# Kernel optimization log

Hardware: AMD Instinct MI355X
Metric: run time of the kernel (lower is better)

The kernel has to match this reference:

```python
import jax, jax.numpy as jnp
import numpy as np

B, T, D_MODEL, HEAD_DIM = 8, 2048, 1024, 128


def setup_inputs() -> dict:
    key = jax.random.key(0)
    k1, k2, k3, k4 = jax.random.split(key, 4)
    scale = 1.0 / np.sqrt(D_MODEL)
    return {
        "x": jax.random.normal(k1, (B, T, D_MODEL), dtype=jnp.float32),
        "Wq": jax.random.normal(k2, (HEAD_DIM, D_MODEL), dtype=jnp.float32) * scale,
        "Wk": jax.random.normal(k3, (HEAD_DIM, D_MODEL), dtype=jnp.float32) * scale,
        "Wv": jax.random.normal(k4, (HEAD_DIM, D_MODEL), dtype=jnp.float32) * scale,
    }


def reference(x, Wq, Wk, Wv) -> jnp.ndarray:
    # x: [B, T, C]; torch Linear(no bias): y = x @ W.T, W: [head_dim, d_model]
    q = jnp.einsum("btc,hc->bth", x, Wq)  # [B, T, H]
    k = jnp.einsum("btc,hc->bth", x, Wk)
    v = jnp.einsum("btc,hc->bth", x, Wv)
    head_dim = Wq.shape[0]
    scores = jnp.einsum("bqh,bkh->bqk", q, k) / jnp.sqrt(jnp.float32(head_dim))  # [B, T, T]
    T_ = x.shape[1]
    causal = jnp.tril(jnp.ones((T_, T_), dtype=bool))
    scores = jnp.where(causal, scores, -jnp.inf)
    probs = jax.nn.softmax(scores, axis=-1)
    # dropout is identity at inference (eval mode)
    out = jnp.einsum("bqk,bkh->bqh", probs, v)  # [B, T, head_dim]
    return out
```

## Files before the change

kernel.cpp:

```cpp
#include <hip/hip_runtime.h>
#include <hip/hip_bf16.h>
#include <math.h>

#define T_ 2048
#define C_ 1024
#define H_ 128
#define NB 8
#define WN 131072
#define SC 0.08838834764831845f

typedef __attribute__((ext_vector_type(8))) short bf16x8;
typedef __attribute__((ext_vector_type(8))) unsigned short u16x8;
typedef __attribute__((ext_vector_type(4))) float f32x4;

#define MFMA16(a,b,c) __builtin_amdgcn_mfma_f32_16x16x32_bf16((a),(b),(c),0,0,0)

__device__ __forceinline__ unsigned short f2bf(float f) {
    union { float f; unsigned u; } v; v.f = f;
    unsigned r = v.u + 0x7fffu + ((v.u >> 16) & 1u);
    return (unsigned short)(r >> 16);
}
__device__ __forceinline__ float bf2f(unsigned short u) {
    union { unsigned u; float f; } v; v.u = ((unsigned)u) << 16; return v.f;
}
__device__ __forceinline__ unsigned pk2bf(float a, float b) {
    __hip_bfloat162 h = __float22bfloat162_rn(float2{a, b});
    union { __hip_bfloat162 h; unsigned u; } v; v.h = h; return v.u;
}
__device__ __forceinline__ void gld16(void* lds, const void* g) {
    __builtin_amdgcn_global_load_lds(
        (const __attribute__((address_space(1))) unsigned*)g,
        (__attribute__((address_space(3))) unsigned*)lds, 16, 0, 0);
}

__global__ __launch_bounds__(256) void wconv(const float* __restrict__ Wq,
                                             const float* __restrict__ Wk,
                                             const float* __restrict__ Wv,
                                             unsigned short* __restrict__ Wb) {
    int e = (blockIdx.x * 256 + threadIdx.x) * 8;
    int which = e >> 17;
    int off = e & (WN - 1);
    const float* src = (which == 0) ? Wq : (which == 1 ? Wk : Wv);
    float s = (which == 0) ? SC : 1.0f;
    const float4* p = (const float4*)(src + off);
    float4 a = p[0], b = p[1];
    uint4 o = { pk2bf(a.x * s, a.y * s), pk2bf(a.z * s, a.w * s),
                pk2bf(b.x * s, b.y * s), pk2bf(b.z * s, b.w * s) };
    *(uint4*)(Wb + e) = o;
}

__global__ __launch_bounds__(256, 2) void proj(const float* __restrict__ x,
                                               const unsigned short* __restrict__ Wb,
                                               unsigned short* __restrict__ Q,
                                               unsigned short* __restrict__ K,
                                               unsigned short* __restrict__ V) {
    __shared__ unsigned short Xs[2][64][64];
    __shared__ unsigned short Ws[2][192][64];

    const int tid  = threadIdx.x;
    const int wave = tid >> 6, lane = tid & 63;
    const int quad = lane >> 4, l16 = lane & 15;
    const int wm   = wave >> 1, wn = wave & 1;
    const int m0   = (blockIdx.x >> 1) * 64;
    const int n0   = (blockIdx.x & 1) * 192;

    f32x4 acc[2][6];
    #pragma unroll
    for (int i = 0; i < 2; i++)
        #pragma unroll
        for (int j = 0; j < 6; j++) acc[i][j] = {0.f, 0.f, 0.f, 0.f};

    const int xrow = tid >> 2, xcg = tid & 3;
    const float* xg = x + (size_t)(m0 + xrow) * C_ + xcg * 16;
    const int xk = xrow & 7;
    const unsigned short* wg = Wb + (size_t)(n0 + wave * 48 + (lane >> 3)) * C_
                               + (size_t)(((lane & 7) ^ (lane >> 3)) * 8);

    float4 xr0, xr1, xr2, xr3;
    #define ISSUE(buf, kc) do {                                                   \
        _Pragma("unroll")                                                         \
        for (int i = 0; i < 6; i++)                                               \
            gld16(&Ws[buf][wave * 48 + i * 8][0], wg + (size_t)i * 8 * C_ + (kc));\
        const float* xp = xg + (kc);                                              \
        xr0 = *(const float4*)xp;        xr1 = *(const float4*)(xp + 4);          \
        xr2 = *(const float4*)(xp + 8);  xr3 = *(const float4*)(xp + 12);         \
    } while (0)

    #define XWRITE(buf) do {                                                      \
        uint4 u0 = { pk2bf(xr0.x, xr0.y), pk2bf(xr0.z, xr0.w),                    \
                     pk2bf(xr1.x, xr1.y), pk2bf(xr1.z, xr1.w) };                  \
        uint4 u1 = { pk2bf(xr2.x, xr2.y), pk2bf(xr2.z, xr2.w),                    \
                     pk2bf(xr3.x, xr3.y), pk2bf(xr3.z, xr3.w) };                  \
        *(uint4*)&Xs[buf][xrow][((2 * xcg)     ^ xk) * 8] = u0;                   \
        *(uint4*)&Xs[buf][xrow][((2 * xcg + 1) ^ xk) * 8] = u1;                   \
    } while (0)

    ISSUE(0, 0);
    XWRITE(0);
    for (int it = 0; it < 16; it++) {
        __syncthreads();
        const int buf = it & 1;
        if (it < 15) ISSUE(buf ^ 1, (it + 1) * 64);
        const int key = l16 & 7;
        bf16x8 af[2][2];
        #pragma unroll
        for (int kk = 0; kk < 2; kk++)
            #pragma unroll
            for (int mf = 0; mf < 2; mf++)
                af[mf][kk] = *(bf16x8*)&Xs[buf][wm * 32 + mf * 16 + l16]
                                          [((kk * 4 + quad) ^ key) * 8];
        #pragma unroll
        for (int kk = 0; kk < 2; kk++)
            #pragma unroll
            for (int nf = 0; nf < 6; nf++) {
                bf16x8 bq = *(bf16x8*)&Ws[buf][wn * 96 + nf * 16 + l16]
                                         [((kk * 4 + quad) ^ key) * 8];
                acc[0][nf] = MFMA16(af[0][kk], bq, acc[0][nf]);
                acc[1][nf] = MFMA16(af[1][kk], bq, acc[1][nf]);
            }
        if (it < 15) XWRITE(buf ^ 1);
    }
    #undef ISSUE
    #undef XWRITE

    #pragma unroll
    for (int nf = 0; nf < 6; nf++) {
        int nb = n0 + wn * 96 + nf * 16;
        int which = nb >> 7;
        unsigned short* dst = (which == 0) ? Q : (which == 1 ? K : V);
        int c = (nb & 127) + l16;
        #pragma unroll
        for (int mf = 0; mf < 2; mf++)
            #pragma unroll
            for (int r = 0; r < 4; r++)
                dst[(size_t)(m0 + wm * 32 + mf * 16 + quad * 4 + r) * H_ + c] = f2bf(acc[mf][nf][r]);
    }
}

__global__ __launch_bounds__(256, 3) void attn(const unsigned short* __restrict__ Qg,
                                               const unsigned short* __restrict__ Kg,
                                               const unsigned short* __restrict__ Vg,
                                               unsigned short* __restrict__ Ob,
                                               float* __restrict__ Ml) {
    const int bid = blockIdx.x;
    const int b   = bid & 7;
    const int j   = bid >> 3;
    int g = 0;
    while (j >= 2 * (g + 1) * (g + 2)) g++;
    const int within = j - 2 * g * (g + 1);
    const int t = within / (g + 1);
    const int s = within - t * (g + 1);
    const int qt = 4 * g + t;
    const int qbase = qt * 64, kstart = s * 256;
    const int kend  = (kstart + 256 < qbase + 64) ? kstart + 256 : qbase + 64;
    const int niter = (kend - kstart) >> 6;

    __shared__ unsigned short Ks[4][64][32];
    __shared__ unsigned short Vt[128 * 64];
    __shared__ unsigned short Ps[4][16][64];

    const int tid = threadIdx.x, wave = tid >> 6, lane = tid & 63;
    const int quad = lane >> 4, l16 = lane & 15;
    const size_t base = (size_t)b * T_ * H_;

    const unsigned short* ksrc = Kg + base + (size_t)(kstart + (lane >> 2)) * H_ + wave * 32 + (lane & 3) * 8;
    #pragma unroll
    for (int p = 0; p < 4; p++) gld16(&Ks[wave][p * 16][0], ksrc + (size_t)p * 16 * H_);
    const unsigned short* vsrc = Vg + base + (size_t)(kstart + wave * 8 + quad * 2) * H_ + l16 * 8;
    u16x8 vr[2][2];
    vr[0][0] = *(const u16x8*)vsrc;             vr[0][1] = *(const u16x8*)(vsrc + H_);
    vr[1][0] = *(const u16x8*)(vsrc + 32 * H_); vr[1][1] = *(const u16x8*)(vsrc + 33 * H_);

    bf16x8 qf[4];
    const unsigned short* qp = Qg + base + (size_t)(qbase + wave * 16 + l16) * H_ + quad * 8;
    #pragma unroll
    for (int kk = 0; kk < 4; kk++) qf[kk] = *(const bf16x8*)(qp + kk * 32);

    f32x4 o[8];
    #pragma unroll
    for (int i = 0; i < 8; i++) o[i] = {0.f, 0.f, 0.f, 0.f};
    float m_i = -INFINITY, l_i = 0.f;
    const int swz = (l16 & 7) << 3;
    const int qg = qbase + wave * 16 + l16;

    __syncthreads();

    #pragma unroll
    for (int g2 = 0; g2 < 2; g2++) {
        int t0 = wave * 8 + g2 * 32 + quad * 2;
        int t8 = t0 >> 3;
        #pragma unroll
        for (int jj = 0; jj < 8; jj++) {
            int h = l16 * 8 + jj;
            unsigned pk = (unsigned)(unsigned short)vr[g2][0][jj] | ((unsigned)(unsigned short)vr[g2][1][jj] << 16);
            int blk = (t8 ^ (h & 7) ^ ((h >> 3) & 7)) & 7;
            *(unsigned*)&Vt[h * 64 + blk * 8 + (t0 & 7)] = pk;
        }
    }

    for (int kt = 0; ; kt++) {
        const int kbase = kstart + kt * 64;
        f32x4 st[4];
        #pragma unroll
        for (int nf = 0; nf < 4; nf++) st[nf] = {0.f, 0.f, 0.f, 0.f};
        #pragma unroll
        for (int kk = 0; kk < 4; kk++)
            #pragma unroll
            for (int nf = 0; nf < 4; nf++) {
                bf16x8 kfr = *(bf16x8*)&Ks[kk][nf * 16 + l16][quad * 8];
                st[nf] = MFMA16(kfr, qf[kk], st[nf]);
            }
        if (kbase + 64 > qbase) {
            #pragma unroll
            for (int nf = 0; nf < 4; nf++) {
                int kg = kbase + nf * 16 + quad * 4;
                #pragma unroll
                for (int r = 0; r < 4; r++)
                    if (kg + r > qg) st[nf][r] = -INFINITY;
            }
        }
        float mx = st[0][0];
        #pragma unroll
        for (int nf = 0; nf < 4; nf++)
            #pragma unroll
            for (int r = 0; r < 4; r++) mx = fmaxf(mx, st[nf][r]);
        mx = fmaxf(mx, __shfl_xor(mx, 16, 64));
        mx = fmaxf(mx, __shfl_xor(mx, 32, 64));
        float mnew = fmaxf(m_i, mx);
        float al = __expf(m_i - mnew);
        m_i = mnew;
        float rs = 0.f;
        #pragma unroll
        for (int nf = 0; nf < 4; nf++)
            #pragma unroll
            for (int r = 0; r < 4; r++) {
                float e = __expf(st[nf][r] - mnew);
                st[nf][r] = e; rs += e;
            }
        rs += __shfl_xor(rs, 16, 64);
        rs += __shfl_xor(rs, 32, 64);
        l_i = al * l_i + rs;
        #pragma unroll
        for (int nf = 0; nf < 4; nf++) {
            uint2 pk = { pk2bf(st[nf][0], st[nf][1]), pk2bf(st[nf][2], st[nf][3]) };
            *(uint2*)&Ps[wave][l16][(nf * 16 + quad * 4) ^ swz] = pk;
        }
        float a0 = __shfl(al, quad * 4 + 0, 64), a1 = __shfl(al, quad * 4 + 1, 64);
        float a2 = __shfl(al, quad * 4 + 2, 64), a3 = __shfl(al, quad * 4 + 3, 64);
        #pragma unroll
        for (int i = 0; i < 8; i++) {
            o[i][0] *= a0; o[i][1] *= a1; o[i][2] *= a2; o[i][3] *= a3;
        }
        __syncthreads();

        const bool more = (kt + 1 < niter);
        if (more) {
            ksrc += 64 * H_;
            #pragma unroll
            for (int p = 0; p < 4; p++) gld16(&Ks[wave][p * 16][0], ksrc + (size_t)p * 16 * H_);
            vsrc += 64 * H_;
            vr[0][0] = *(const u16x8*)vsrc;             vr[0][1] = *(const u16x8*)(vsrc + H_);
            vr[1][0] = *(const u16x8*)(vsrc + 32 * H_); vr[1][1] = *(const u16x8*)(vsrc + 33 * H_);
        }
        bf16x8 pa0 = *(bf16x8*)&Ps[wave][l16][(quad * 8) ^ swz];
        bf16x8 pa1 = *(bf16x8*)&Ps[wave][l16][(32 + quad * 8) ^ swz];
        #pragma unroll
        for (int nf = 0; nf < 8; nf++) {
            int h = nf * 16 + l16;
            int ex = (h & 7) ^ ((h >> 3) & 7);
            bf16x8 v0 = *(bf16x8*)&Vt[h * 64 + ((quad ^ ex) & 7) * 8];
            bf16x8 v1 = *(bf16x8*)&Vt[h * 64 + (((quad + 4) ^ ex) & 7) * 8];
            o[nf] = MFMA16(pa0, v0, o[nf]);
            o[nf] = MFMA16(pa1, v1, o[nf]);
        }
        if (!more) break;
        __syncthreads();
        #pragma unroll
        for (int g2 = 0; g2 < 2; g2++) {
            int t0 = wave * 8 + g2 * 32 + quad * 2;
            int t8 = t0 >> 3;
            #pragma unroll
            for (int jj = 0; jj < 8; jj++) {
                int h = l16 * 8 + jj;
                unsigned pk = (unsigned)(unsigned short)vr[g2][0][jj] | ((unsigned)(unsigned short)vr[g2][1][jj] << 16);
                int blk = (t8 ^ (h & 7) ^ ((h >> 3) & 7)) & 7;
                *(unsigned*)&Vt[h * 64 + blk * 8 + (t0 & 7)] = pk;
            }
        }
    }

    const int slot = j * NB + b;
    float lq[4];
    #pragma unroll
    for (int r = 0; r < 4; r++) lq[r] = __shfl(l_i, quad * 4 + r, 64);
    const size_t obase = (size_t)slot * 64 * 128;
    #pragma unroll
    for (int r = 0; r < 4; r++) {
        float invl = 1.0f / lq[r];
        #pragma unroll
        for (int nf = 0; nf < 8; nf++)
            Ob[obase + (size_t)(wave * 16 + quad * 4 + r) * 128 + nf * 16 + l16] = f2bf(o[nf][r] * invl);
    }
    if (lane < 16) {
        int ridx = slot * 64 + wave * 16 + l16;
        Ml[ridx * 2]     = m_i;
        Ml[ridx * 2 + 1] = l_i;
    }
}

__global__ __launch_bounds__(256) void merge(const unsigned short* __restrict__ Ob,
                                             const float* __restrict__ Ml,
                                             float* __restrict__ out) {
    const int qt = blockIdx.x, b = blockIdx.y;
    const int g = qt >> 2;
    const int Pq = 2 * g * (g + 1) + (qt & 3) * (g + 1);
    const int ns = g + 1;
    const int tid = threadIdx.x;
    const int row = tid >> 2, c0 = (tid & 3) * 32;

    float mv[8], lv[8], mg = -INFINITY;
    for (int s2 = 0; s2 < ns; s2++) {
        int slot = (Pq + s2) * NB + b;
        mv[s2] = Ml[(slot * 64 + row) * 2];
        lv[s2] = Ml[(slot * 64 + row) * 2 + 1];
        mg = fmaxf(mg, mv[s2]);
    }
    float L = 0.f, w[8];
    for (int s2 = 0; s2 < ns; s2++) { w[s2] = lv[s2] * __expf(mv[s2] - mg); L += w[s2]; }
    float inv = 1.0f / L;

    float accv[32];
    #pragma unroll
    for (int i = 0; i < 32; i++) accv[i] = 0.f;
    for (int s2 = 0; s2 < ns; s2++) {
        int slot = (Pq + s2) * NB + b;
        const unsigned short* op = Ob + ((size_t)(slot * 64 + row)) * 128 + c0;
        #pragma unroll
        for (int cc = 0; cc < 4; cc++) {
            u16x8 v = *(const u16x8*)(op + cc * 8);
            #pragma unroll
            for (int jj = 0; jj < 8; jj++) accv[cc * 8 + jj] += w[s2] * bf2f(v[jj]);
        }
    }
    float* od = out + ((size_t)(b * T_ + qt * 64 + row)) * 128 + c0;
    #pragma unroll
    for (int cc = 0; cc < 8; cc++) {
        float4 w4 = { accv[cc*4] * inv, accv[cc*4+1] * inv, accv[cc*4+2] * inv, accv[cc*4+3] * inv };
        *(float4*)(od + cc * 4) = w4;
    }
}

extern "C" void kernel_launch(void* const* d_in, const int* in_sizes, int n_in,
                              void* d_out, int out_size, void* d_ws, size_t ws_size,
                              hipStream_t stream) {
    const float* x  = (const float*)d_in[0];
    const float* Wq = (const float*)d_in[1];
    const float* Wk = (const float*)d_in[2];
    const float* Wv = (const float*)d_in[3];

    char* ws = (char*)d_ws;
    unsigned short* Wb = (unsigned short*)ws;
    unsigned short* Q  = (unsigned short*)(ws + (size_t) 1 * (1u << 20));
    unsigned short* K  = (unsigned short*)(ws + (size_t) 5 * (1u << 20));
    unsigned short* V  = (unsigned short*)(ws + (size_t) 9 * (1u << 20));
    unsigned short* Ob = (unsigned short*)(ws + (size_t)13 * (1u << 20));
    float*          Ml = (float*)(ws + (size_t)32 * (1u << 20));
    float* out = (float*)d_out;

    hipLaunchKernelGGL(wconv, dim3(192), dim3(256), 0, stream, Wq, Wk, Wv, Wb);
    hipLaunchKernelGGL(proj,  dim3(512), dim3(256), 0, stream, x, Wb, Q, K, V);
    hipLaunchKernelGGL(attn,  dim3(1152), dim3(256), 0, stream, Q, K, V, Ob, Ml);
    hipLaunchKernelGGL(merge, dim3(32, NB), dim3(256), 0, stream, Ob, Ml, out);
}
```

Before: 166.2 us.

## Deepen QKV projection pipeline with two x register buffers and partial vmcnt waits

Restructures the QKV projection GEMM main loop so x global loads run two k-steps ahead using two register buffers, while W async loads target LDS one step ahead. Replaces __syncthreads with explicit s_waitcnt vmcnt(4) plus s_barrier and sched_barrier pins, so the wait covers only the older loads. The aim is to hide global load latency behind MFMA work. It costs extra registers and depends on hand-counted vmcnt values matching the order in which loads are issued.

```diff
diff --git a/kernel.cpp b/kernel.cpp
--- a/kernel.cpp
+++ b/kernel.cpp
@@ -73,55 +73,98 @@
     const int xrow = tid >> 2, xcg = tid & 3;
     const float* xg = x + (size_t)(m0 + xrow) * C_ + xcg * 16;
     const int xk = xrow & 7;
+    const int key = l16 & 7;
     const unsigned short* wg = Wb + (size_t)(n0 + wave * 48 + (lane >> 3)) * C_
                                + (size_t)(((lane & 7) ^ (lane >> 3)) * 8);
 
-    float4 xr0, xr1, xr2, xr3;
-    #define ISSUE(buf, kc) do {                                                   \
+    float4 xA[4], xB[4];
+
+    #define WISSUE(buf, kc) do {                                                  \
         _Pragma("unroll")                                                         \
         for (int i = 0; i < 6; i++)                                               \
             gld16(&Ws[buf][wave * 48 + i * 8][0], wg + (size_t)i * 8 * C_ + (kc));\
+    } while (0)
+
+    #define XLOAD(dst, kc) do {                                                   \
         const float* xp = xg + (kc);                                              \
-        xr0 = *(const float4*)xp;        xr1 = *(const float4*)(xp + 4);          \
-        xr2 = *(const float4*)(xp + 8);  xr3 = *(const float4*)(xp + 12);         \
-    } while (0)
-
-    #define XWRITE(buf) do {                                                      \
-        uint4 u0 = { pk2bf(xr0.x, xr0.y), pk2bf(xr0.z, xr0.w),                    \
-                     pk2bf(xr1.x, xr1.y), pk2bf(xr1.z, xr1.w) };                  \
-        uint4 u1 = { pk2bf(xr2.x, xr2.y), pk2bf(xr2.z, xr2.w),                    \
-                     pk2bf(xr3.x, xr3.y), pk2bf(xr3.z, xr3.w) };                  \
+        dst[0] = *(const float4*)xp;        dst[1] = *(const float4*)(xp + 4);    \
+        dst[2] = *(const float4*)(xp + 8);  dst[3] = *(const float4*)(xp + 12);   \
+    } while (0)
+
+    #define XWR(buf, src) do {                                                    \
+        uint4 u0 = { pk2bf(src[0].x, src[0].y), pk2bf(src[0].z, src[0].w),        \
+                     pk2bf(src[1].x, src[1].y), pk2bf(src[1].z, src[1].w) };      \
+        uint4 u1 = { pk2bf(src[2].x, src[2].y), pk2bf(src[2].z, src[2].w),        \
+                     pk2bf(src[3].x, src[3].y), pk2bf(src[3].z, src[3].w) };      \
         *(uint4*)&Xs[buf][xrow][((2 * xcg)     ^ xk) * 8] = u0;                   \
         *(uint4*)&Xs[buf][xrow][((2 * xcg + 1) ^ xk) * 8] = u1;                   \
     } while (0)
 
-    ISSUE(0, 0);
-    XWRITE(0);
-    for (int it = 0; it < 16; it++) {
-        __syncthreads();
-        const int buf = it & 1;
-        if (it < 15) ISSUE(buf ^ 1, (it + 1) * 64);
-        const int key = l16 & 7;
-        bf16x8 af[2][2];
-        #pragma unroll
-        for (int kk = 0; kk < 2; kk++)
-            #pragma unroll
-            for (int mf = 0; mf < 2; mf++)
-                af[mf][kk] = *(bf16x8*)&Xs[buf][wm * 32 + mf * 16 + l16]
-                                          [((kk * 4 + quad) ^ key) * 8];
-        #pragma unroll
-        for (int kk = 0; kk < 2; kk++)
-            #pragma unroll
-            for (int nf = 0; nf < 6; nf++) {
-                bf16x8 bq = *(bf16x8*)&Ws[buf][wn * 96 + nf * 16 + l16]
-                                         [((kk * 4 + quad) ^ key) * 8];
-                acc[0][nf] = MFMA16(af[0][kk], bq, acc[0][nf]);
-                acc[1][nf] = MFMA16(af[1][kk], bq, acc[1][nf]);
-            }
-        if (it < 15) XWRITE(buf ^ 1);
-    }
-    #undef ISSUE
-    #undef XWRITE
+    #define COMPUTE(buf) do {                                                     \
+        bf16x8 af[2][2];                                                          \
+        _Pragma("unroll")                                                         \
+        for (int kk = 0; kk < 2; kk++)                                            \
+            _Pragma("unroll")                                                     \
+            for (int mf = 0; mf < 2; mf++)                                        \
+                af[mf][kk] = *(bf16x8*)&Xs[buf][wm * 32 + mf * 16 + l16]          \
+                                          [((kk * 4 + quad) ^ key) * 8];          \
+        _Pragma("unroll")                                                         \
+        for (int kk = 0; kk < 2; kk++)                                            \
+            _Pragma("unroll")                                                     \
+            for (int nf = 0; nf < 6; nf++) {                                      \
+                bf16x8 bq = *(bf16x8*)&Ws[buf][wn * 96 + nf * 16 + l16]           \
+                                         [((kk * 4 + quad) ^ key) * 8];           \
+                acc[0][nf] = MFMA16(af[0][kk], bq, acc[0][nf]);                   \
+                acc[1][nf] = MFMA16(af[1][kk], bq, acc[1][nf]);                   \
+            }                                                                     \
+    } while (0)
+
+    #define BAR4 do {                                                             \
+        asm volatile("s_waitcnt vmcnt(4) lgkmcnt(0)" ::: "memory");               \
+        __builtin_amdgcn_s_barrier();                                             \
+        __builtin_amdgcn_sched_barrier(0);                                        \
+    } while (0)
+    #define BAR0 do {                                                             \
+        asm volatile("s_waitcnt vmcnt(0) lgkmcnt(0)" ::: "memory");               \
+        __builtin_amdgcn_s_barrier();                                             \
+        __builtin_amdgcn_sched_barrier(0);                                        \
+    } while (0)
+    #define PIN __builtin_amdgcn_sched_barrier(0)
+
+    XLOAD(xA, 0);
+    WISSUE(0, 0);
+    PIN;
+    XLOAD(xB, 64);
+    XWR(0, xA);
+
+    for (int t = 0; t < 7; t++) {
+        BAR4;
+        WISSUE(1, (2 * t + 1) * 64);
+        PIN;
+        XLOAD(xA, (2 * t + 2) * 64);
+        COMPUTE(0);
+        XWR(1, xB);
+        BAR4;
+        WISSUE(0, (2 * t + 2) * 64);
+        PIN;
+        XLOAD(xB, (2 * t + 3) * 64);
+        COMPUTE(1);
+        XWR(0, xA);
+    }
+    BAR4;
+    WISSUE(1, 15 * 64);
+    COMPUTE(0);
+    XWR(1, xB);
+    BAR0;
+    COMPUTE(1);
+
+    #undef WISSUE
+    #undef XLOAD
+    #undef XWR
+    #undef COMPUTE
+    #undef BAR4
+    #undef BAR0
+    #undef PIN
 
     #pragma unroll
     for (int nf = 0; nf < 6; nf++) {
```

Measured after the change: 159.4 us. 1.04x faster.
